# Kernel optimization log

Measured on AMD Instinct MI355X. Metric: run time of the kernel, lower is better.

The kernel has to match this reference:

```python
import jax, jax.numpy as jnp
import numpy as np

R = 16            # search_range
D = 2 * R + 1     # 33 offsets per axis -> 1089 cost channels
B, C, H, W = 64, 256, 16, 16
OUT = 512         # conv channels for search_range=16
FULLY = 1024
EPS_BN = 1e-5
EPS_NORM = 1e-12
LRELU_SLOPE = 0.01


def l2_normalize(x):
    # torch F.normalize(x, dim=1, p=2): x / clamp_min(||x||_2, 1e-12)
    n = jnp.sqrt(jnp.sum(x * x, axis=1, keepdims=True))
    return x / jnp.maximum(n, EPS_NORM)


def cost_volume(c1, warp, r):
    # Fused equivalent of the original (2r+1)^2 Python-loop of slice/mul/mean:
    # one dense correlation GEMM over the padded map, then a gather of the
    # diagonal-band entries. cost[b,dy,dx,i,j] = mean_c c1[b,c,i,j]*pad[b,c,i+dy,j+dx]
    b, c, h, w = c1.shape
    d = 2 * r + 1
    padded = jnp.pad(warp, ((0, 0), (0, 0), (r, r), (r, r)))          # (B,C,h+2r,w+2r)
    full = jnp.einsum('bcij,bcuv->bijuv', c1, padded) / c             # (B,h,w,h+2r,w+2r)
    dy = jnp.arange(d)
    ii = jnp.arange(h)
    jj = jnp.arange(w)
    I = ii[None, None, :, None]                 # (1,1,h,1)
    J = jj[None, None, None, :]                 # (1,1,1,w)
    U = dy[:, None, None, None] + I             # (d,1,h,1)
    V = dy[None, :, None, None] + J             # (1,d,1,w)
    cost = full[:, I, J, U, V]                  # (B,d,d,h,w)
    cost = cost.reshape(b, d * d, h, w)
    return jnp.where(cost > 0, cost, LRELU_SLOPE * cost)  # LeakyReLU(0.01)


def conv_bn_relu(x, Wc, bc, g, be, stride):
    y = jax.lax.conv_general_dilated(
        x, Wc, window_strides=(stride, stride), padding=((1, 1), (1, 1)),
        dimension_numbers=('NCHW', 'OIHW', 'NCHW'))
    y = y + bc[None, :, None, None]
    # training-mode BatchNorm: biased batch stats over (B,H,W)
    mu = jnp.mean(y, axis=(0, 2, 3), keepdims=True)
    var = jnp.var(y, axis=(0, 2, 3), keepdims=True)
    y = (y - mu) * jax.lax.rsqrt(var + EPS_BN)
    y = y * g[None, :, None, None] + be[None, :, None, None]
    return jnp.maximum(y, 0.0)


def setup_inputs() -> dict:
    key = jax.random.key(0)
    ks = jax.random.split(key, 10)
    s = 0.02
    inp = {
        'feature1': jax.random.normal(ks[0], (B, C, H, W), jnp.float32),
        'feature2': jax.random.normal(ks[1], (B, C, H, W), jnp.float32),
        'W1': jax.random.normal(ks[2], (OUT, D * D, 3, 3), jnp.float32) * s,
        'b1': jnp.zeros((OUT,), jnp.float32),
        'g1': jnp.ones((OUT,), jnp.float32),
        'be1': jnp.zeros((OUT,), jnp.float32),
        'W2': jax.random.normal(ks[3], (OUT, OUT, 3, 3), jnp.float32) * s,
        'b2': jnp.zeros((OUT,), jnp.float32),
        'g2': jnp.ones((OUT,), jnp.float32),
        'be2': jnp.zeros((OUT,), jnp.float32),
        'W3': jax.random.normal(ks[4], (OUT, OUT, 3, 3), jnp.float32) * s,
        'b3': jnp.zeros((OUT,), jnp.float32),
        'g3': jnp.ones((OUT,), jnp.float32),
        'be3': jnp.zeros((OUT,), jnp.float32),
        'Wf1': jax.random.normal(ks[5], (FULLY, 256 * OUT), jnp.float32) * s,
        'bf1': jnp.zeros((FULLY,), jnp.float32),
        'Wf2': jax.random.normal(ks[6], (8, FULLY), jnp.float32) * s,
        'bf2': jnp.zeros((8,), jnp.float32),
    }
    return inp


def reference(feature1, feature2, W1, b1, g1, be1, W2, b2, g2, be2,
              W3, b3, g3, be3, Wf1, bf1, Wf2, bf2):
    # warped=False: normalize both feature maps
    gc = cost_volume(l2_normalize(feature1), l2_normalize(feature2), R)
    x = conv_bn_relu(gc, W1, b1, g1, be1, 1)
    x = conv_bn_relu(x, W2, b2, g2, be2, 1)
    x = conv_bn_relu(x, W3, b3, g3, be3, 1)
    x = x.reshape(x.shape[0], -1)               # (B, 512*16*16)
    x = jnp.maximum(x @ Wf1.T + bf1, 0.0)       # Linear + ReLU
    # Dropout treated as identity (deterministic reference)
    offset = x @ Wf2.T + bf2                    # (B, 8)
    return offset
```

## Files before the change

### kernel.cpp

```cpp
#include <hip/hip_runtime.h>
#include <hip/hip_bf16.h>
#include <stdint.h>


typedef unsigned short ushort_t;
typedef __attribute__((ext_vector_type(8))) short     bf16x8;
typedef __attribute__((ext_vector_type(8))) unsigned short u16x8;
typedef __attribute__((ext_vector_type(2))) unsigned short u16x2;
typedef __attribute__((ext_vector_type(4))) float     f32x4;

#define NB   64
#define NC   256
#define NP   256
#define KP1  1152
#define NOUT 512
#define NROWS 16384
#define KFC  131072
#define NF   1024
#define KSPL 32

__device__ __forceinline__ unsigned short f2bf(float x) {
  union { float f; unsigned u; } c; c.f = x;
  unsigned r = c.u + 0x7FFFu + ((c.u >> 16) & 1u);
  return (unsigned short)(r >> 16);
}
__device__ __forceinline__ float b2f(unsigned short u) {
  union { unsigned u; float f; } c; c.u = ((unsigned)u) << 16; return c.f;
}

__device__ __forceinline__ void gl_lds16(const void* g, void* l) {
  __builtin_amdgcn_global_load_lds(
      (const __attribute__((address_space(1))) unsigned int*)g,
      (__attribute__((address_space(3))) unsigned int*)l, 16, 0, 0);
}

__device__ __forceinline__ f32x4 mfma16(bf16x8 a, bf16x8 b, f32x4 c) {
  return __builtin_amdgcn_mfma_f32_16x16x32_bf16(a, b, c, 0, 0, 0);
}

__global__ __launch_bounds__(1024) void l2norm_t(
    const float* __restrict__ f1, const float* __restrict__ f2,
    ushort_t* __restrict__ AT, ushort_t* __restrict__ N2T)
{
  __shared__ float red[4][256];
  const float* src = blockIdx.y ? f2 : f1;
  ushort_t*    dst = blockIdx.y ? N2T : AT;
  const int b = blockIdx.x;
  const int pos = threadIdx.x & 255, q = threadIdx.x >> 8;
  const float* sb = src + (size_t)b * NC * NP;
  float sq = 0.f;
  for (int c = q * 64; c < q * 64 + 64; ++c) {
    float v = sb[c * NP + pos]; sq += v * v;
  }
  red[q][pos] = sq;
  __syncthreads();
  float tot = red[0][pos] + red[1][pos] + red[2][pos] + red[3][pos];
  float sc = 1.f / fmaxf(sqrtf(tot), 1e-12f);
  ushort_t* db = dst + ((size_t)b * NP + pos) * NC;
#pragma unroll
  for (int j = 0; j < 8; ++j) {
    int c0 = q * 64 + j * 8;
    u16x8 pk;
#pragma unroll
    for (int k = 0; k < 8; ++k) pk[k] = f2bf(sb[(c0 + k) * NP + pos] * sc);
    *(u16x8*)(db + c0) = pk;
  }
}

#define T1P (9 * NOUT * KP1)
#define T23 (9 * NOUT * 512)
__global__ __launch_bounds__(256) void pack_all(
    const float* __restrict__ W1, const float* __restrict__ W2,
    const float* __restrict__ W3, ushort_t* __restrict__ Wp1,
    ushort_t* __restrict__ Wp2, ushort_t* __restrict__ Wp3)
{
  int p = blockIdx.x * 256 + threadIdx.x;
  const float* W; ushort_t* Wp; int Cin, Kp, q;
  if (p < T1P)            { W = W1; Wp = Wp1; Cin = 1089; Kp = KP1; q = p; }
  else if (p < T1P + T23) { W = W2; Wp = Wp2; Cin = 512;  Kp = 512; q = p - T1P; }
  else if (p < T1P + 2 * T23) { W = W3; Wp = Wp3; Cin = 512; Kp = 512; q = p - T1P - T23; }
  else return;
  int tap = q / (NOUT * Kp);
  int rem = q - tap * (NOUT * Kp);
  int o   = rem / Kp;
  int cin = rem - o * Kp;
  float v = (cin < Cin) ? W[((size_t)o * Cin + cin) * 9 + tap] : 0.f;
  Wp[q] = f2bf(v);
}

__global__ __launch_bounds__(256) void corr_gemm(
    const ushort_t* __restrict__ AT,
    const ushort_t* __restrict__ N2T,
    float* __restrict__ C)
{
  __shared__ ushort_t As[128 * 64];
  __shared__ ushort_t Bs[128 * 64];
  const int tid = threadIdx.x, lane = tid & 63, wave = tid >> 6;
  const int wr = wave >> 1, wc = wave & 1;
  const int la = lane & 15, lb = lane >> 4;
  const int b  = blockIdx.z;
  const int m0 = blockIdx.y * 128;
  const int n0 = blockIdx.x * 128;

  f32x4 acc[4][4];
#pragma unroll
  for (int i = 0; i < 4; ++i)
#pragma unroll
    for (int j = 0; j < 4; ++j) acc[i][j] = (f32x4){0.f, 0.f, 0.f, 0.f};

  const ushort_t* srcA[4];
  const ushort_t* srcB[4];
#pragma unroll
  for (int s = 0; s < 4; ++s) {
    int idx = tid + (s << 8);
    int row = idx >> 3, c16 = idx & 7;
    srcA[s] = AT  + ((size_t)b * NP + m0 + row) * NC + c16 * 8;
    srcB[s] = N2T + ((size_t)b * NP + n0 + row) * NC + c16 * 8;
  }

  for (int kc = 0; kc < NC; kc += 64) {
#pragma unroll
    for (int s = 0; s < 4; ++s) {
      int idx = tid + (s << 8);
      gl_lds16(srcA[s] + kc, &As[idx * 8]);
      gl_lds16(srcB[s] + kc, &Bs[idx * 8]);
    }
    __syncthreads();
#pragma unroll
    for (int kk = 0; kk < 2; ++kk) {
      bf16x8 af[4], bfv[4];
#pragma unroll
      for (int mi = 0; mi < 4; ++mi)
        af[mi] = *(const bf16x8*)&As[(wr * 64 + mi * 16 + la) * 64 + kk * 32 + lb * 8];
#pragma unroll
      for (int ni = 0; ni < 4; ++ni)
        bfv[ni] = *(const bf16x8*)&Bs[(wc * 64 + ni * 16 + la) * 64 + kk * 32 + lb * 8];
#pragma unroll
      for (int mi = 0; mi < 4; ++mi)
#pragma unroll
        for (int ni = 0; ni < 4; ++ni)
          acc[mi][ni] = mfma16(af[mi], bfv[ni], acc[mi][ni]);
    }
    __syncthreads();
  }

#pragma unroll
  for (int ni = 0; ni < 4; ++ni) {
    int col = n0 + wc * 64 + ni * 16 + la;
#pragma unroll
    for (int mi = 0; mi < 4; ++mi) {
      int p = m0 + wr * 64 + mi * 16 + lb * 4;
#pragma unroll
      for (int r = 0; r < 4; ++r)
        C[((size_t)b * NP + p + r) * NP + col] = acc[mi][ni][r];
    }
  }
}

__global__ __launch_bounds__(576) void cost_write(
    const float* __restrict__ C, ushort_t* __restrict__ costT)
{
  __shared__ float row[256];
  const int ij = blockIdx.x, b = blockIdx.y, tid = threadIdx.x;
  const float* cr = C + ((size_t)b * NP + ij) * NP;
  if (tid < 256) row[tid] = cr[tid];
  __syncthreads();
  const int i = ij >> 4, j = ij & 15;
  const int d0 = tid * 2;
  u16x2 pk;
#pragma unroll
  for (int q = 0; q < 2; ++q) {
    int dd = d0 + q;
    int dy = dd / 33;
    int dx = dd - dy * 33;
    int oi = dy + i - 16, oj = dx + j - 16;
    float v = 0.f;
    if (((unsigned)oi < 16u) & ((unsigned)oj < 16u))
      v = row[oi * 16 + oj] * (1.f / 256.f);
    v = v > 0.f ? v : 0.01f * v;
    pk[q] = f2bf(v);
  }
  *(u16x2*)(costT + ((size_t)b * NP + ij) * KP1 + d0) = pk;
}

__global__ __launch_bounds__(512, 1) void conv_gemm256(
    const ushort_t* __restrict__ X, const ushort_t* __restrict__ Wp,
    const float* __restrict__ bias, ushort_t* __restrict__ Y0,
    ushort_t* __restrict__ Y1, const int K, const int TPT, const int NT2,
    const ushort_t* __restrict__ zerot)
{
  __shared__ ushort_t lds[65536];
  const int tid = threadIdx.x;
  const int lane = tid & 63, wave = tid >> 6;
  const int wr = wave >> 2, wc = wave & 3;
  const int la = lane & 15, lb = lane >> 4;

  const int bid = blockIdx.x;
  const int L = ((bid & 7) << 5) + (bid >> 3);
  const int g = L >> 7;
  const int rem = L & 127;
  const int b = rem >> 1;
  const int n0 = (rem & 1) << 8;
  const int t0 = g * NT2;

  int amask[4];
  const ushort_t* abase[4];
  const ushort_t* bbase[4];
#pragma unroll
  for (int s = 0; s < 4; ++s) {
    int idx = tid + (s << 9);
    int ks = idx & 7, loc = (idx >> 3) & 63;
    int rA = ((s & 1) << 7) + ((s >> 1) << 6) + loc;
    int i = rA >> 4, j = rA & 15;
    int m = 0;
#pragma unroll
    for (int tap = 0; tap < 9; ++tap) {
      int i2 = i + tap / 3 - 1, j2 = j + tap % 3 - 1;
      if (((unsigned)i2 < 16u) & ((unsigned)j2 < 16u)) m |= 1 << tap;
    }
    amask[s] = m;
    abase[s] = X + (size_t)(b * NP + rA) * K + ((ks ^ (rA & 7)) << 3);
    int rB = ((s & 1) << 7) + ((loc >> 5) << 6) + ((s >> 1) << 5) + (loc & 31);
    bbase[s] = Wp + (size_t)(n0 + rB) * K + ((ks ^ (rB & 7)) << 3);
  }

  const int ck0 = ((0 + lb) ^ (la & 7)) << 3;
  const int ck1 = ((4 + lb) ^ (la & 7)) << 3;
  const int a_base = wr * 4096 + la * 64;
  const int b_base = 16384 + (wc >> 1) * 4096 + (wc & 1) * 2048 + la * 64;

  f32x4 acc[8][4];
#pragma unroll
  for (int i = 0; i < 8; ++i)
#pragma unroll
    for (int j = 0; j < 4; ++j) acc[i][j] = (f32x4){0.f, 0.f, 0.f, 0.f};

  auto tile_par = [&](int tg, int& toffA, size_t& wtap, int& tap) {
    tap = tg / TPT;
    int kc = (tg - tap * TPT) << 6;
    int ty = tap / 3;
    toffA = (ty * 16 + (tap - 3 * ty) - 17) * K + kc;
    wtap  = (size_t)tap * NOUT * K + kc;
  };

#define STAGE_A(S) { const ushort_t* gp = ((amask[S] >> tapN) & 1) ? abase[S] + toffN : zerot; \
                     gl_lds16(gp, &bufn[(tid + ((S) << 9)) * 8]); }
#define STAGE_B(S) gl_lds16(bbase[S] + wtapN, &bufn[16384 + (tid + ((S) << 9)) * 8]);

#define READ_A03() \
  Af[0][0] = *(const bf16x8*)&buf[a_base + 0    + ck0]; Af[0][1] = *(const bf16x8*)&buf[a_base + 0    + ck1]; \
  Af[1][0] = *(const bf16x8*)&buf[a_base + 1024 + ck0]; Af[1][1] = *(const bf16x8*)&buf[a_base + 1024 + ck1]; \
  Af[2][0] = *(const bf16x8*)&buf[a_base + 2048 + ck0]; Af[2][1] = *(const bf16x8*)&buf[a_base + 2048 + ck1]; \
  Af[3][0] = *(const bf16x8*)&buf[a_base + 3072 + ck0]; Af[3][1] = *(const bf16x8*)&buf[a_base + 3072 + ck1];
#define READ_A47() \
  Af[4][0] = *(const bf16x8*)&buf[a_base + 8192 + 0    + ck0]; Af[4][1] = *(const bf16x8*)&buf[a_base + 8192 + 0    + ck1]; \
  Af[5][0] = *(const bf16x8*)&buf[a_base + 8192 + 1024 + ck0]; Af[5][1] = *(const bf16x8*)&buf[a_base + 8192 + 1024 + ck1]; \
  Af[6][0] = *(const bf16x8*)&buf[a_base + 8192 + 2048 + ck0]; Af[6][1] = *(const bf16x8*)&buf[a_base + 8192 + 2048 + ck1]; \
  Af[7][0] = *(const bf16x8*)&buf[a_base + 8192 + 3072 + ck0]; Af[7][1] = *(const bf16x8*)&buf[a_base + 8192 + 3072 + ck1];
#define READ_B(NOFF) \
  bf00 = *(const bf16x8*)&buf[b_base + (NOFF) + 0    + ck0]; bf01 = *(const bf16x8*)&buf[b_base + (NOFF) + 0    + ck1]; \
  bf10 = *(const bf16x8*)&buf[b_base + (NOFF) + 1024 + ck0]; bf11 = *(const bf16x8*)&buf[b_base + (NOFF) + 1024 + ck1];
#define MFMA_QUAD(MB, N0, N1) \
  acc[MB+0][N0] = mfma16(Af[MB+0][0], bf00, acc[MB+0][N0]); \
  acc[MB+0][N1] = mfma16(Af[MB+0][0], bf10, acc[MB+0][N1]); \
  acc[MB+1][N0] = mfma16(Af[MB+1][0], bf00, acc[MB+1][N0]); \
  acc[MB+1][N1] = mfma16(Af[MB+1][0], bf10, acc[MB+1][N1]); \
  acc[MB+2][N0] = mfma16(Af[MB+2][0], bf00, acc[MB+2][N0]); \
  acc[MB+2][N1] = mfma16(Af[MB+2][0], bf10, acc[MB+2][N1]); \
  acc[MB+3][N0] = mfma16(Af[MB+3][0], bf00, acc[MB+3][N0]); \
  acc[MB+3][N1] = mfma16(Af[MB+3][0], bf10, acc[MB+3][N1]); \
  acc[MB+0][N0] = mfma16(Af[MB+0][1], bf01, acc[MB+0][N0]); \
  acc[MB+0][N1] = mfma16(Af[MB+0][1], bf11, acc[MB+0][N1]); \
  acc[MB+1][N0] = mfma16(Af[MB+1][1], bf01, acc[MB+1][N0]); \
  acc[MB+1][N1] = mfma16(Af[MB+1][1], bf11, acc[MB+1][N1]); \
  acc[MB+2][N0] = mfma16(Af[MB+2][1], bf01, acc[MB+2][N0]); \
  acc[MB+2][N1] = mfma16(Af[MB+2][1], bf11, acc[MB+2][N1]); \
  acc[MB+3][N0] = mfma16(Af[MB+3][1], bf01, acc[MB+3][N0]); \
  acc[MB+3][N1] = mfma16(Af[MB+3][1], bf11, acc[MB+3][N1]);

  {
    ushort_t* bufn = &lds[0];
    int tapN, toffN; size_t wtapN;
    tile_par(t0, toffN, wtapN, tapN);
    STAGE_A(0) STAGE_A(1) STAGE_A(2) STAGE_A(3)
    STAGE_B(0) STAGE_B(1) STAGE_B(2) STAGE_B(3)
  }
  asm volatile("s_waitcnt vmcnt(2)" ::: "memory");
  __builtin_amdgcn_s_barrier();

  bf16x8 Af[8][2];

  for (int t = 0; t < NT2 - 1; ++t) {
    const ushort_t* buf = &lds[(t & 1) << 15];
    ushort_t* bufn = &lds[((t + 1) & 1) << 15];
    int tapN, toffN; size_t wtapN;
    tile_par(t0 + t + 1, toffN, wtapN, tapN);
    bf16x8 bf00, bf01, bf10, bf11;

    READ_A03()
    READ_B(0)
    STAGE_A(0) STAGE_A(1)
    asm volatile("s_waitcnt vmcnt(6)" ::: "memory");
    __builtin_amdgcn_s_barrier();
    asm volatile("s_waitcnt lgkmcnt(0)" ::: "memory");
    __builtin_amdgcn_sched_barrier(0);
    __builtin_amdgcn_s_setprio(1);
    MFMA_QUAD(0, 0, 1)
    __builtin_amdgcn_s_setprio(0);

    READ_A47()
    READ_B(0)
    STAGE_A(2) STAGE_A(3)
    asm volatile("s_waitcnt vmcnt(4)" ::: "memory");
    __builtin_amdgcn_s_barrier();
    asm volatile("s_waitcnt lgkmcnt(0)" ::: "memory");
    __builtin_amdgcn_sched_barrier(0);
    __builtin_amdgcn_s_setprio(1);
    MFMA_QUAD(4, 0, 1)
    __builtin_amdgcn_s_setprio(0);

    READ_B(8192)
    STAGE_B(0) STAGE_B(1)
    __builtin_amdgcn_s_barrier();
    asm volatile("s_waitcnt lgkmcnt(0)" ::: "memory");
    __builtin_amdgcn_sched_barrier(0);
    __builtin_amdgcn_s_setprio(1);
    MFMA_QUAD(0, 2, 3)
    __builtin_amdgcn_s_setprio(0);

    READ_B(8192)
    STAGE_B(2) STAGE_B(3)
    asm volatile("s_waitcnt vmcnt(2)" ::: "memory");
    __builtin_amdgcn_s_barrier();
    asm volatile("s_waitcnt lgkmcnt(0)" ::: "memory");
    __builtin_amdgcn_sched_barrier(0);
    __builtin_amdgcn_s_setprio(1);
    MFMA_QUAD(4, 2, 3)
    __builtin_amdgcn_s_setprio(0);
  }

  {
    const ushort_t* buf = &lds[((NT2 - 1) & 1) << 15];
    bf16x8 bf00, bf01, bf10, bf11;
    asm volatile("s_waitcnt vmcnt(0)" ::: "memory");
    __builtin_amdgcn_s_barrier();
    READ_A03()
    READ_B(0)
    asm volatile("s_waitcnt lgkmcnt(0)" ::: "memory");
    __builtin_amdgcn_sched_barrier(0);
    MFMA_QUAD(0, 0, 1)
    READ_A47()
    asm volatile("s_waitcnt lgkmcnt(0)" ::: "memory");
    __builtin_amdgcn_sched_barrier(0);
    MFMA_QUAD(4, 0, 1)
    READ_B(8192)
    asm volatile("s_waitcnt lgkmcnt(0)" ::: "memory");
    __builtin_amdgcn_sched_barrier(0);
    MFMA_QUAD(0, 2, 3)
    MFMA_QUAD(4, 2, 3)
  }

  ushort_t* Yh = g ? Y1 : Y0;
#pragma unroll
  for (int ni = 0; ni < 4; ++ni) {
    int col = n0 + wc * 64 + ni * 16 + la;
    float bv = 0.5f * bias[col];
#pragma unroll
    for (int mi = 0; mi < 8; ++mi) {
      int row = b * NP + wr * 128 + mi * 16 + lb * 4;
#pragma unroll
      for (int r = 0; r < 4; ++r)
        Yh[(size_t)(row + r) * NOUT + col] = f2bf(acc[mi][ni][r] + bv);
    }
  }
#undef STAGE_A
#undef STAGE_B
#undef READ_A03
#undef READ_A47
#undef READ_B
#undef MFMA_QUAD
}

__global__ __launch_bounds__(512, 1) void conv_fused(
    const ushort_t* __restrict__ X, const ushort_t* __restrict__ Wp,
    const float* __restrict__ bias, ushort_t* __restrict__ Y,
    float* __restrict__ st, const int K, const int TPT, const int NT,
    const ushort_t* __restrict__ zerot)
{
  __shared__ ushort_t lds[2 * 24576];
  const int tid = threadIdx.x;
  const int lane = tid & 63, wave = tid >> 6;
  const int wr = wave >> 2, wc = wave & 3;
  const int la = lane & 15, lb = lane >> 4;

  const int bid = blockIdx.x;
  const int L = ((bid & 7) << 5) + (bid >> 3);
  const int b = L >> 2;
  const int n0 = (L & 3) << 7;

  int amask[4];
  const ushort_t* abase[4];
  const ushort_t* bbase[2];
#pragma unroll
  for (int s = 0; s < 4; ++s) {
    int idx = tid + (s << 9);
    int ks = idx & 7, loc = (idx >> 3) & 63;
    int rA = ((s & 1) << 7) + ((s >> 1) << 6) + loc;
    int i = rA >> 4, j = rA & 15;
    int m = 0;
#pragma unroll
    for (int tap = 0; tap < 9; ++tap) {
      int i2 = i + tap / 3 - 1, j2 = j + tap % 3 - 1;
      if (((unsigned)i2 < 16u) & ((unsigned)j2 < 16u)) m |= 1 << tap;
    }
    amask[s] = m;
    abase[s] = X + (size_t)(b * NP + rA) * K + ((ks ^ (rA & 7)) << 3);
  }
#pragma unroll
  for (int s = 0; s < 2; ++s) {
    int idx = tid + (s << 9);
    int ks = idx & 7, loc = (idx >> 3) & 63;
    int rB = (s << 6) + loc;
    bbase[s] = Wp + (size_t)(n0 + rB) * K + ((ks ^ (rB & 7)) << 3);
  }

  const int ck0 = ((0 + lb) ^ (la & 7)) << 3;
  const int ck1 = ((4 + lb) ^ (la & 7)) << 3;
  const int a_base = wr * 4096 + la * 64;
  const int b_off  = 16384 + (wc * 32 + la) * 64;

  f32x4 acc[8][2];
#pragma unroll
  for (int i = 0; i < 8; ++i)
#pragma unroll
    for (int j = 0; j < 2; ++j) acc[i][j] = (f32x4){0.f, 0.f, 0.f, 0.f};

  auto tile_par = [&](int tg, int& toffA, size_t& wtap, int& tap) {
    tap = tg / TPT;
    int kc = (tg - tap * TPT) << 6;
    int ty = tap / 3;
    toffA = (ty * 16 + (tap - 3 * ty) - 17) * K + kc;
    wtap  = (size_t)tap * NOUT * K + kc;
  };

#define FSTAGE_A(S) { const ushort_t* gp = ((amask[S] >> tapN) & 1) ? abase[S] + toffN : zerot; \
                      gl_lds16(gp, &bufn[(tid + ((S) << 9)) * 8]); }
#define FSTAGE_B(S) gl_lds16(bbase[S] + wtapN, &bufn[16384 + (tid + ((S) << 9)) * 8]);
#define FREAD_A03() \
  Af[0][0] = *(const bf16x8*)&buf[a_base + 0    + ck0]; Af[0][1] = *(const bf16x8*)&buf[a_base + 0    + ck1]; \
  Af[1][0] = *(const bf16x8*)&buf[a_base + 1024 + ck0]; Af[1][1] = *(const bf16x8*)&buf[a_base + 1024 + ck1]; \
  Af[2][0] = *(const bf16x8*)&buf[a_base + 2048 + ck0]; Af[2][1] = *(const bf16x8*)&buf[a_base + 2048 + ck1]; \
  Af[3][0] = *(const bf16x8*)&buf[a_base + 3072 + ck0]; Af[3][1] = *(const bf16x8*)&buf[a_base + 3072 + ck1];
#define FREAD_A47() \
  Af[0][0] = *(const bf16x8*)&buf[a_base + 8192 + 0    + ck0]; Af[0][1] = *(const bf16x8*)&buf[a_base + 8192 + 0    + ck1]; \
  Af[1][0] = *(const bf16x8*)&buf[a_base + 8192 + 1024 + ck0]; Af[1][1] = *(const bf16x8*)&buf[a_base + 8192 + 1024 + ck1]; \
  Af[2][0] = *(const bf16x8*)&buf[a_base + 8192 + 2048 + ck0]; Af[2][1] = *(const bf16x8*)&buf[a_base + 8192 + 2048 + ck1]; \
  Af[3][0] = *(const bf16x8*)&buf[a_base + 8192 + 3072 + ck0]; Af[3][1] = *(const bf16x8*)&buf[a_base + 8192 + 3072 + ck1];
#define FREAD_B() \
  Bf[0][0] = *(const bf16x8*)&buf[b_off + 0    + ck0]; Bf[0][1] = *(const bf16x8*)&buf[b_off + 0    + ck1]; \
  Bf[1][0] = *(const bf16x8*)&buf[b_off + 1024 + ck0]; Bf[1][1] = *(const bf16x8*)&buf[b_off + 1024 + ck1];
#define FMFMA(AB) \
  acc[(AB)+0][0] = mfma16(Af[0][0], Bf[0][0], acc[(AB)+0][0]); \
  acc[(AB)+0][1] = mfma16(Af[0][0], Bf[1][0], acc[(AB)+0][1]); \
  acc[(AB)+1][0] = mfma16(Af[1][0], Bf[0][0], acc[(AB)+1][0]); \
  acc[(AB)+1][1] = mfma16(Af[1][0], Bf[1][0], acc[(AB)+1][1]); \
  acc[(AB)+2][0] = mfma16(Af[2][0], Bf[0][0], acc[(AB)+2][0]); \
  acc[(AB)+2][1] = mfma16(Af[2][0], Bf[1][0], acc[(AB)+2][1]); \
  acc[(AB)+3][0] = mfma16(Af[3][0], Bf[0][0], acc[(AB)+3][0]); \
  acc[(AB)+3][1] = mfma16(Af[3][0], Bf[1][0], acc[(AB)+3][1]); \
  acc[(AB)+0][0] = mfma16(Af[0][1], Bf[0][1], acc[(AB)+0][0]); \
  acc[(AB)+0][1] = mfma16(Af[0][1], Bf[1][1], acc[(AB)+0][1]); \
  acc[(AB)+1][0] = mfma16(Af[1][1], Bf[0][1], acc[(AB)+1][0]); \
  acc[(AB)+1][1] = mfma16(Af[1][1], Bf[1][1], acc[(AB)+1][1]); \
  acc[(AB)+2][0] = mfma16(Af[2][1], Bf[0][1], acc[(AB)+2][0]); \
  acc[(AB)+2][1] = mfma16(Af[2][1], Bf[1][1], acc[(AB)+2][1]); \
  acc[(AB)+3][0] = mfma16(Af[3][1], Bf[0][1], acc[(AB)+3][0]); \
  acc[(AB)+3][1] = mfma16(Af[3][1], Bf[1][1], acc[(AB)+3][1]);

  {
    ushort_t* bufn = &lds[0];
    int tapN, toffN; size_t wtapN;
    tile_par(0, toffN, wtapN, tapN);
    FSTAGE_A(0) FSTAGE_A(1) FSTAGE_B(0) FSTAGE_B(1) FSTAGE_A(2) FSTAGE_A(3)
  }
  asm volatile("s_waitcnt vmcnt(2)" ::: "memory");
  __builtin_amdgcn_s_barrier();

  for (int t = 0; t < NT - 1; ++t) {
    const ushort_t* buf = &lds[(t & 1) * 24576];
    ushort_t* bufn = &lds[((t + 1) & 1) * 24576];
    int tapN, toffN; size_t wtapN;
    tile_par(t + 1, toffN, wtapN, tapN);
    bf16x8 Af[4][2], Bf[2][2];

    FREAD_A03()
    FREAD_B()
    FSTAGE_A(0) FSTAGE_A(1) FSTAGE_B(0) FSTAGE_B(1)
    asm volatile("s_waitcnt vmcnt(4)" ::: "memory");
    __builtin_amdgcn_s_barrier();
    asm volatile("s_waitcnt lgkmcnt(0)" ::: "memory");
    __builtin_amdgcn_sched_barrier(0);
    __builtin_amdgcn_s_setprio(1);
    FMFMA(0)
    __builtin_amdgcn_s_setprio(0);

    FREAD_A47()
    FSTAGE_A(2) FSTAGE_A(3)
    asm volatile("s_waitcnt vmcnt(2)" ::: "memory");
    __builtin_amdgcn_s_barrier();
    asm volatile("s_waitcnt lgkmcnt(0)" ::: "memory");
    __builtin_amdgcn_sched_barrier(0);
    __builtin_amdgcn_s_setprio(1);
    FMFMA(4)
    __builtin_amdgcn_s_setprio(0);
  }

  {
    const ushort_t* buf = &lds[((NT - 1) & 1) * 24576];
    bf16x8 Af[4][2], Bf[2][2];
    FREAD_A03()
    FREAD_B()
    asm volatile("s_waitcnt vmcnt(0)" ::: "memory");
    __builtin_amdgcn_s_barrier();
    asm volatile("s_waitcnt lgkmcnt(0)" ::: "memory");
    __builtin_amdgcn_sched_barrier(0);
    FMFMA(0)
    FREAD_A47()
    asm volatile("s_waitcnt lgkmcnt(0)" ::: "memory");
    __builtin_amdgcn_sched_barrier(0);
    FMFMA(4)
  }

#pragma unroll
  for (int ni = 0; ni < 2; ++ni) {
    int col = n0 + wc * 32 + ni * 16 + la;
    float bv = bias[col];
    float s = 0.f, qq = 0.f;
#pragma unroll
    for (int mi = 0; mi < 8; ++mi) {
      int row = b * NP + wr * 128 + mi * 16 + lb * 4;
#pragma unroll
      for (int r = 0; r < 4; ++r) {
        float v = acc[mi][ni][r] + bv;
        Y[(size_t)(row + r) * NOUT + col] = f2bf(v);
        s += v; qq += v * v;
      }
    }
    s  += __shfl_xor(s, 16);  s  += __shfl_xor(s, 32);
    qq += __shfl_xor(qq, 16); qq += __shfl_xor(qq, 32);
    if (lb == 0) {
      atomicAdd(&st[col], s);
      atomicAdd(&st[512 + col], qq);
    }
  }
#undef FSTAGE_A
#undef FSTAGE_B
#undef FREAD_A03
#undef FREAD_A47
#undef FREAD_B
#undef FMFMA
}

__global__ __launch_bounds__(512) void bn_stat2(
    const ushort_t* __restrict__ Y0, const ushort_t* __restrict__ Y1,
    float* __restrict__ st)
{
  __shared__ float ls[8][64][8];
  __shared__ float lq[8][64][8];
  const int tid = threadIdx.x;
  const int cg = tid & 63, rr = tid >> 6;
  const size_t base = (size_t)blockIdx.x * 32 * NOUT;
  float s8[8], q8[8];
#pragma unroll
  for (int j = 0; j < 8; ++j) { s8[j] = 0.f; q8[j] = 0.f; }
  for (int k = 0; k < 4; ++k) {
    size_t off = base + (size_t)(rr * 4 + k) * NOUT + cg * 8;
    u16x8 a = *(const u16x8*)(Y0 + off);
    u16x8 c = *(const u16x8*)(Y1 + off);
#pragma unroll
    for (int j = 0; j < 8; ++j) {
      float y = b2f(a[j]) + b2f(c[j]);
      s8[j] += y; q8[j] += y * y;
    }
  }
#pragma unroll
  for (int j = 0; j < 8; ++j) { ls[rr][cg][j] = s8[j]; lq[rr][cg][j] = q8[j]; }
  __syncthreads();
  const int cg2 = tid >> 3, j2 = tid & 7;
  float s = 0.f, q = 0.f;
#pragma unroll
  for (int r = 0; r < 8; ++r) { s += ls[r][cg2][j2]; q += lq[r][cg2][j2]; }
  atomicAdd(&st[cg2 * 8 + j2], s);
  atomicAdd(&st[512 + cg2 * 8 + j2], q);
}

__global__ __launch_bounds__(256) void bn_apply2(
    const ushort_t* __restrict__ Y0, const ushort_t* __restrict__ Y1,
    const float* __restrict__ st, const float* __restrict__ g,
    const float* __restrict__ be, ushort_t* __restrict__ Xo)
{
  const size_t idx = (size_t)blockIdx.x * 256 + threadIdx.x;
  u16x8 a = *(const u16x8*)(Y0 + idx * 8);
  u16x8 c = *(const u16x8*)(Y1 + idx * 8);
  const int c0 = (int)((idx * 8) & 511);
  u16x8 pk;
#pragma unroll
  for (int q = 0; q < 8; ++q) {
    int cc = c0 + q;
    float y = b2f(a[q]) + b2f(c[q]);
    float mu  = st[cc] * (1.f / 16384.f);
    float var = st[512 + cc] * (1.f / 16384.f) - mu * mu;
    float s = rsqrtf(var + 1e-5f) * g[cc];
    pk[q] = f2bf(fmaxf((y - mu) * s + be[cc], 0.f));
  }
  *(u16x8*)(Xo + idx * 8) = pk;
}

__global__ __launch_bounds__(256) void bn_apply_s(
    const ushort_t* __restrict__ Y, const float* __restrict__ st,
    const float* __restrict__ g, const float* __restrict__ be,
    ushort_t* __restrict__ Xo)
{
  const size_t idx = (size_t)blockIdx.x * 256 + threadIdx.x;
  u16x8 a = *(const u16x8*)(Y + idx * 8);
  const int c0 = (int)((idx * 8) & 511);
  u16x8 pk;
#pragma unroll
  for (int q = 0; q < 8; ++q) {
    int cc = c0 + q;
    float y = b2f(a[q]);
    float mu  = st[cc] * (1.f / 16384.f);
    float var = st[512 + cc] * (1.f / 16384.f) - mu * mu;
    float s = rsqrtf(var + 1e-5f) * g[cc];
    pk[q] = f2bf(fmaxf((y - mu) * s + be[cc], 0.f));
  }
  *(u16x8*)(Xo + idx * 8) = pk;
}

__global__ __launch_bounds__(256) void bn_apply_ts(
    const ushort_t* __restrict__ Y, const float* __restrict__ st,
    const float* __restrict__ g, const float* __restrict__ be,
    ushort_t* __restrict__ Xf)
{
  __shared__ ushort_t T[64][65];
  const int c0  = blockIdx.x * 64;
  const int ij0 = blockIdx.y * 64;
  const int b   = blockIdx.z;
  const int tid = threadIdx.x;

#pragma unroll
  for (int it = 0; it < 16; ++it) {
    int e = it * 256 + tid;
    int ij = e >> 6, c = e & 63;
    int cg = c0 + c;
    float y = b2f(Y[((size_t)(b * NP + ij0 + ij)) * NOUT + cg]);
    float mu  = st[cg] * (1.f / 16384.f);
    float var = st[512 + cg] * (1.f / 16384.f) - mu * mu;
    float s = rsqrtf(var + 1e-5f) * g[cg];
    T[ij][c] = f2bf(fmaxf((y - mu) * s + be[cg], 0.f));
  }
  __syncthreads();
#pragma unroll
  for (int it = 0; it < 16; ++it) {
    int e = it * 256 + tid;
    int cr = e >> 6, ijc = e & 63;
    Xf[(size_t)b * KFC + (size_t)(c0 + cr) * NP + ij0 + ijc] = T[ijc][cr];
  }
}

__device__ __forceinline__ u16x8 pack8(float4 a, float4 b) {
  u16x8 r;
  r[0] = f2bf(a.x); r[1] = f2bf(a.y); r[2] = f2bf(a.z); r[3] = f2bf(a.w);
  r[4] = f2bf(b.x); r[5] = f2bf(b.y); r[6] = f2bf(b.z); r[7] = f2bf(b.w);
  return r;
}

__global__ __launch_bounds__(256) void fc1_gemm(
    const ushort_t* __restrict__ Xf, const float* __restrict__ Wf1,
    float* __restrict__ hacc)
{
  __shared__ ushort_t As[64 * 64];
  __shared__ ushort_t Bs[64 * 64];
  const int tid = threadIdx.x, lane = tid & 63, wave = tid >> 6;
  const int la = lane & 15, lb = lane >> 4;
  const int f0 = blockIdx.x * 64;
  const int k0 = blockIdx.y * 4096;

  f32x4 acc[4];
#pragma unroll
  for (int i = 0; i < 4; ++i) acc[i] = (f32x4){0.f, 0.f, 0.f, 0.f};

  const ushort_t* xrow[2];
#pragma unroll
  for (int s = 0; s < 2; ++s) {
    int idx = tid + (s << 8);
    xrow[s] = Xf + (size_t)(idx >> 3) * KFC + k0 + (idx & 7) * 8;
  }
  const int brow = tid >> 2, kseg = (tid & 3) * 16;
  const float* wrow = Wf1 + (size_t)(f0 + brow) * KFC + k0 + kseg;

  for (int kc = 0; kc < 4096; kc += 64) {
#pragma unroll
    for (int s = 0; s < 2; ++s) {
      int idx = tid + (s << 8);
      gl_lds16(xrow[s] + kc, &As[idx * 8]);
    }
    float4 w0 = *(const float4*)(wrow + kc);
    float4 w1 = *(const float4*)(wrow + kc + 4);
    float4 w2 = *(const float4*)(wrow + kc + 8);
    float4 w3 = *(const float4*)(wrow + kc + 12);
    *(u16x8*)&Bs[brow * 64 + kseg]     = pack8(w0, w1);
    *(u16x8*)&Bs[brow * 64 + kseg + 8] = pack8(w2, w3);
    __syncthreads();
#pragma unroll
    for (int kk = 0; kk < 2; ++kk) {
      bf16x8 bfv = *(const bf16x8*)&Bs[(wave * 16 + la) * 64 + kk * 32 + lb * 8];
#pragma unroll
      for (int mi = 0; mi < 4; ++mi) {
        bf16x8 av = *(const bf16x8*)&As[(mi * 16 + la) * 64 + kk * 32 + lb * 8];
        acc[mi] = mfma16(av, bfv, acc[mi]);
      }
    }
    __syncthreads();
  }

  float* slice = hacc + (size_t)blockIdx.y * NB * NF;
#pragma unroll
  for (int mi = 0; mi < 4; ++mi) {
    int row = mi * 16 + lb * 4;
#pragma unroll
    for (int r = 0; r < 4; ++r)
      slice[(size_t)(row + r) * NF + f0 + wave * 16 + la] = acc[mi][r];
  }
}

__global__ __launch_bounds__(256) void fc2_out(
    const float* __restrict__ hacc, const float* __restrict__ bf1,
    const float* __restrict__ Wf2, const float* __restrict__ bf2,
    float* __restrict__ out)
{
  const int b = blockIdx.x, tid = threadIdx.x;
  float a[8];
#pragma unroll
  for (int o = 0; o < 8; ++o) a[o] = 0.f;
  for (int f = tid; f < NF; f += 256) {
    float hv = bf1[f];
#pragma unroll 4
    for (int s = 0; s < KSPL; ++s)
      hv += hacc[((size_t)s * NB + b) * NF + f];
    hv = fmaxf(hv, 0.f);
#pragma unroll
    for (int o = 0; o < 8; ++o) a[o] += hv * Wf2[o * NF + f];
  }
  __shared__ float red[8][256];
#pragma unroll
  for (int o = 0; o < 8; ++o) red[o][tid] = a[o];
  __syncthreads();
  for (int s = 128; s > 0; s >>= 1) {
    if (tid < s) {
#pragma unroll
      for (int o = 0; o < 8; ++o) red[o][tid] += red[o][tid + s];
    }
    __syncthreads();
  }
  if (tid < 8) out[b * 8 + tid] = red[tid][0] + bf2[tid];
}

extern "C" void kernel_launch(void* const* d_in, const int* in_sizes, int n_in,
                              void* d_out, int out_size, void* d_ws, size_t ws_size,
                              hipStream_t stream) {
  const float* f1  = (const float*)d_in[0];
  const float* f2  = (const float*)d_in[1];
  const float* W1  = (const float*)d_in[2];
  const float* b1  = (const float*)d_in[3];
  const float* g1  = (const float*)d_in[4];
  const float* be1 = (const float*)d_in[5];
  const float* W2  = (const float*)d_in[6];
  const float* b2  = (const float*)d_in[7];
  const float* g2  = (const float*)d_in[8];
  const float* be2 = (const float*)d_in[9];
  const float* W3  = (const float*)d_in[10];
  const float* b3  = (const float*)d_in[11];
  const float* g3  = (const float*)d_in[12];
  const float* be3 = (const float*)d_in[13];
  const float* Wf1 = (const float*)d_in[14];
  const float* bf1 = (const float*)d_in[15];
  const float* Wf2 = (const float*)d_in[16];
  const float* bf2 = (const float*)d_in[17];
  float* out = (float*)d_out;

  char* ws = (char*)d_ws;
  size_t off = 0;
  auto alloc = [&](size_t bytes) -> void* {
    void* p = ws + off;
    off += (bytes + 255) & ~(size_t)255;
    return p;
  };

  ushort_t* zerot = (ushort_t*)alloc(256);
  float* st1  = (float*)alloc(1024 * 4);
  float* st2  = (float*)alloc(1024 * 4);
  float* st3  = (float*)alloc(1024 * 4);
  const size_t zero_bytes = off;

  float* hacc = (float*)alloc((size_t)KSPL * NB * NF * 4);
  const size_t SZ_AT   = (size_t)NB * NP * NC * 2;
  const size_t SZ_COST = (size_t)NB * NP * KP1 * 2;
  const size_t SZ_WP1  = (size_t)9 * NOUT * KP1 * 2;
  const size_t SZ_WP23 = (size_t)9 * NOUT * 512 * 2;
  ushort_t* AT    = (ushort_t*)alloc(SZ_AT);
  ushort_t* N2T   = (ushort_t*)alloc(SZ_AT);
  float*    Cbuf  = (float*)alloc((size_t)NB * NP * NP * 4);
  ushort_t* costT = (ushort_t*)alloc(SZ_COST);
  ushort_t* Wp1   = (ushort_t*)alloc(SZ_WP1);
  ushort_t* Wp2   = (ushort_t*)alloc(SZ_WP23);
  ushort_t* Wp3   = (ushort_t*)alloc(SZ_WP23);
  ushort_t* Yh0   = (ushort_t*)alloc((size_t)NROWS * NOUT * 2);
  ushort_t* Yh1   = (ushort_t*)alloc((size_t)NROWS * NOUT * 2);
  ushort_t* Xbuf  = (ushort_t*)alloc((size_t)NROWS * NOUT * 2);
  ushort_t* Xf    = (ushort_t*)alloc((size_t)NB * KFC * 2);

  hipMemsetAsync(ws, 0, zero_bytes, stream);

  l2norm_t<<<dim3(64, 2), 1024, 0, stream>>>(f1, f2, AT, N2T);

  pack_all<<<(T1P + 2 * T23 + 255) / 256, 256, 0, stream>>>(W1, W2, W3, Wp1, Wp2, Wp3);

  corr_gemm<<<dim3(2, 2, 64), 256, 0, stream>>>(AT, N2T, Cbuf);
  cost_write<<<dim3(256, 64), 576, 0, stream>>>(Cbuf, costT);

  conv_gemm256<<<256, 512, 0, stream>>>(costT, Wp1, b1, Yh0, Yh1, KP1, 18, 81, zerot);
  bn_stat2<<<512, 512, 0, stream>>>(Yh0, Yh1, st1);
  bn_apply2<<<4096, 256, 0, stream>>>(Yh0, Yh1, st1, g1, be1, Xbuf);

  conv_fused<<<256, 512, 0, stream>>>(Xbuf, Wp2, b2, Yh0, st2, 512, 8, 72, zerot);
  bn_apply_s<<<4096, 256, 0, stream>>>(Yh0, st2, g2, be2, Xbuf);

  conv_fused<<<256, 512, 0, stream>>>(Xbuf, Wp3, b3, Yh0, st3, 512, 8, 72, zerot);
  bn_apply_ts<<<dim3(8, 4, 64), 256, 0, stream>>>(Yh0, st3, g3, be3, Xf);

  fc1_gemm<<<dim3(16, KSPL), 256, 0, stream>>>(Xf, Wf1, hacc);
  fc2_out<<<64, 256, 0, stream>>>(hacc, bf1, Wf2, bf2, out);

  (void)in_sizes; (void)n_in; (void)out_size; (void)ws_size;
}
```

Before: 573.3 us.

## Fuse BatchNorm apply into conv kernels via cooperative grid sync

The two 512-channel conv kernels become cooperative launches. Each block accumulates BN statistics, waits at a grid-wide sync, then applies BN and ReLU straight from its register accumulators. For the last conv it also transposes through LDS into the FC input layout. This drops the bf16 pre-BN intermediate write and re-read, and removes two separate BN-apply kernel launches. In exchange it needs all 256 blocks to be co-resident and adds a grid barrier that stalls every block until the slowest one finishes.

```diff
diff --git a/kernel.cpp b/kernel.cpp
--- a/kernel.cpp
+++ b/kernel.cpp
@@ -1,11 +1,15 @@
 #include <hip/hip_runtime.h>
 #include <hip/hip_bf16.h>
+#include <hip/hip_cooperative_groups.h>
 #include <stdint.h>
 
+
+namespace cg = cooperative_groups;
 
 typedef unsigned short ushort_t;
 typedef __attribute__((ext_vector_type(8))) short     bf16x8;
 typedef __attribute__((ext_vector_type(8))) unsigned short u16x8;
+typedef __attribute__((ext_vector_type(4))) unsigned short u16x4;
 typedef __attribute__((ext_vector_type(2))) unsigned short u16x2;
 typedef __attribute__((ext_vector_type(4))) float     f32x4;
 
@@ -381,11 +385,12 @@
 #undef MFMA_QUAD
 }
 
-__global__ __launch_bounds__(512, 1) void conv_fused(
+__global__ __launch_bounds__(512, 1) void conv_coop(
     const ushort_t* __restrict__ X, const ushort_t* __restrict__ Wp,
-    const float* __restrict__ bias, ushort_t* __restrict__ Y,
-    float* __restrict__ st, const int K, const int TPT, const int NT,
-    const ushort_t* __restrict__ zerot)
+    const float* __restrict__ bias, const float* __restrict__ gam,
+    const float* __restrict__ bet, float* __restrict__ st,
+    ushort_t* __restrict__ Xout, const int K, const int TPT, const int NT,
+    const int tmode, const ushort_t* __restrict__ zerot)
 {
   __shared__ ushort_t lds[2 * 24576];
   const int tid = threadIdx.x;
@@ -537,20 +542,72 @@
     float bv = bias[col];
     float s = 0.f, qq = 0.f;
 #pragma unroll
-    for (int mi = 0; mi < 8; ++mi) {
-      int row = b * NP + wr * 128 + mi * 16 + lb * 4;
+    for (int mi = 0; mi < 8; ++mi)
 #pragma unroll
       for (int r = 0; r < 4; ++r) {
         float v = acc[mi][ni][r] + bv;
-        Y[(size_t)(row + r) * NOUT + col] = f2bf(v);
         s += v; qq += v * v;
       }
-    }
     s  += __shfl_xor(s, 16);  s  += __shfl_xor(s, 32);
     qq += __shfl_xor(qq, 16); qq += __shfl_xor(qq, 32);
     if (lb == 0) {
       atomicAdd(&st[col], s);
       atomicAdd(&st[512 + col], qq);
+    }
+  }
+
+  cg::this_grid().sync();
+
+  if (tmode == 0) {
+#pragma unroll
+    for (int ni = 0; ni < 2; ++ni) {
+      int col = n0 + wc * 32 + ni * 16 + la;
+      float bv = bias[col];
+      float mu  = st[col] * (1.f / 16384.f);
+      float var = st[512 + col] * (1.f / 16384.f) - mu * mu;
+      float sc2 = rsqrtf(var + 1e-5f) * gam[col];
+      float bb  = bet[col];
+#pragma unroll
+      for (int mi = 0; mi < 8; ++mi) {
+        int row = b * NP + wr * 128 + mi * 16 + lb * 4;
+#pragma unroll
+        for (int r = 0; r < 4; ++r) {
+          float v = acc[mi][ni][r] + bv;
+          Xout[(size_t)(row + r) * NOUT + col] =
+              f2bf(fmaxf((v - mu) * sc2 + bb, 0.f));
+        }
+      }
+    }
+  } else {
+    ushort_t* T = &lds[0];
+#pragma unroll
+    for (int ni = 0; ni < 2; ++ni) {
+      int col = n0 + wc * 32 + ni * 16 + la;
+      float bv = bias[col];
+      float mu  = st[col] * (1.f / 16384.f);
+      float var = st[512 + col] * (1.f / 16384.f) - mu * mu;
+      float sc2 = rsqrtf(var + 1e-5f) * gam[col];
+      float bb  = bet[col];
+      int cl = col - n0;
+#pragma unroll
+      for (int mi = 0; mi < 8; ++mi) {
+        int rowl = wr * 128 + mi * 16 + lb * 4;
+        u16x4 pk;
+#pragma unroll
+        for (int r = 0; r < 4; ++r) {
+          float v = acc[mi][ni][r] + bv;
+          pk[r] = f2bf(fmaxf((v - mu) * sc2 + bb, 0.f));
+        }
+        *(u16x4*)&T[cl * 280 + rowl] = pk;
+      }
+    }
+    __syncthreads();
+    ushort_t* dst = Xout + (size_t)b * KFC + (size_t)n0 * NP;
+#pragma unroll
+    for (int it = 0; it < 8; ++it) {
+      int f = it * 4096 + tid * 8;
+      int c = f >> 8, ij = f & 255;
+      *(u16x8*)(dst + f) = *(const u16x8*)&T[c * 280 + ij];
     }
   }
 #undef FSTAGE_A
@@ -614,58 +671,6 @@
     pk[q] = f2bf(fmaxf((y - mu) * s + be[cc], 0.f));
   }
   *(u16x8*)(Xo + idx * 8) = pk;
-}
-
-__global__ __launch_bounds__(256) void bn_apply_s(
-    const ushort_t* __restrict__ Y, const float* __restrict__ st,
-    const float* __restrict__ g, const float* __restrict__ be,
-    ushort_t* __restrict__ Xo)
-{
-  const size_t idx = (size_t)blockIdx.x * 256 + threadIdx.x;
-  u16x8 a = *(const u16x8*)(Y + idx * 8);
-  const int c0 = (int)((idx * 8) & 511);
-  u16x8 pk;
-#pragma unroll
-  for (int q = 0; q < 8; ++q) {
-    int cc = c0 + q;
-    float y = b2f(a[q]);
-    float mu  = st[cc] * (1.f / 16384.f);
-    float var = st[512 + cc] * (1.f / 16384.f) - mu * mu;
-    float s = rsqrtf(var + 1e-5f) * g[cc];
-    pk[q] = f2bf(fmaxf((y - mu) * s + be[cc], 0.f));
-  }
-  *(u16x8*)(Xo + idx * 8) = pk;
-}
-
-__global__ __launch_bounds__(256) void bn_apply_ts(
-    const ushort_t* __restrict__ Y, const float* __restrict__ st,
-    const float* __restrict__ g, const float* __restrict__ be,
-    ushort_t* __restrict__ Xf)
-{
-  __shared__ ushort_t T[64][65];
-  const int c0  = blockIdx.x * 64;
-  const int ij0 = blockIdx.y * 64;
-  const int b   = blockIdx.z;
-  const int tid = threadIdx.x;
-
-#pragma unroll
-  for (int it = 0; it < 16; ++it) {
-    int e = it * 256 + tid;
-    int ij = e >> 6, c = e & 63;
-    int cg = c0 + c;
-    float y = b2f(Y[((size_t)(b * NP + ij0 + ij)) * NOUT + cg]);
-    float mu  = st[cg] * (1.f / 16384.f);
-    float var = st[512 + cg] * (1.f / 16384.f) - mu * mu;
-    float s = rsqrtf(var + 1e-5f) * g[cg];
-    T[ij][c] = f2bf(fmaxf((y - mu) * s + be[cg], 0.f));
-  }
-  __syncthreads();
-#pragma unroll
-  for (int it = 0; it < 16; ++it) {
-    int e = it * 256 + tid;
-    int cr = e >> 6, ijc = e & 63;
-    Xf[(size_t)b * KFC + (size_t)(c0 + cr) * NP + ij0 + ijc] = T[ijc][cr];
-  }
 }
 
 __device__ __forceinline__ u16x8 pack8(float4 a, float4 b) {
@@ -833,11 +838,25 @@
   bn_stat2<<<512, 512, 0, stream>>>(Yh0, Yh1, st1);
   bn_apply2<<<4096, 256, 0, stream>>>(Yh0, Yh1, st1, g1, be1, Xbuf);
 
-  conv_fused<<<256, 512, 0, stream>>>(Xbuf, Wp2, b2, Yh0, st2, 512, 8, 72, zerot);
-  bn_apply_s<<<4096, 256, 0, stream>>>(Yh0, st2, g2, be2, Xbuf);
-
-  conv_fused<<<256, 512, 0, stream>>>(Xbuf, Wp3, b3, Yh0, st3, 512, 8, 72, zerot);
-  bn_apply_ts<<<dim3(8, 4, 64), 256, 0, stream>>>(Yh0, st3, g3, be3, Xf);
+  {
+    const ushort_t* xp = Xbuf; const ushort_t* wpp = Wp2;
+    const float* bp = b2; const float* gp = g2; const float* bep = be2;
+    float* stp = st2; ushort_t* xop = Xbuf;
+    int Kk = 512, tpt = 8, nt = 72, tm = 0;
+    const ushort_t* zp = zerot;
+    void* args[] = {&xp, &wpp, &bp, &gp, &bep, &stp, &xop, &Kk, &tpt, &nt, &tm, &zp};
+    hipLaunchCooperativeKernel((void*)conv_coop, dim3(256), dim3(512), args, 0, stream);
+  }
+
+  {
+    const ushort_t* xp = Xbuf; const ushort_t* wpp = Wp3;
+    const float* bp = b3; const float* gp = g3; const float* bep = be3;
+    float* stp = st3; ushort_t* xop = Xf;
+    int Kk = 512, tpt = 8, nt = 72, tm = 1;
+    const ushort_t* zp = zerot;
+    void* args[] = {&xp, &wpp, &bp, &gp, &bep, &stp, &xop, &Kk, &tpt, &nt, &tm, &zp};
+    hipLaunchCooperativeKernel((void*)conv_coop, dim3(256), dim3(512), args, 0, stream);
+  }
 
   fc1_gemm<<<dim3(16, KSPL), 256, 0, stream>>>(Xf, Wf1, hacc);
   fc2_out<<<64, 256, 0, stream>>>(hacc, bf1, Wf2, bf2, out);
```

New measurement: 625.2 us. +9.1%, slower.
